# Optimization experiments

Measured on AMD Instinct MI355X. Metric: run time of the kernel, lower is better.

## Reference

```python
import jax, jax.numpy as jnp
import numpy as np

N = 100000        # nodes
E = 1_600_000     # edges (before self loops)
G = 512           # graphs in batch
IN = 64           # in_channels
HID = 48          # hidden_channels
H = 4             # heads
C = HID // H      # per-head channels
OUT = 10          # out_channels


def setup_inputs() -> dict:
    key = jax.random.key(0)
    ks = jax.random.split(key, 24)
    s = 0.1
    inp = {
        "x": jax.random.normal(ks[0], (N, IN), jnp.float32),
        "edge_index": jax.random.randint(ks[1], (2, E), 0, N, dtype=jnp.int64),
        "edge_weight": jax.random.uniform(ks[2], (E,), jnp.float32),
        "batch": jnp.sort(jax.random.randint(ks[3], (N,), 0, G, dtype=jnp.int64)),
        # GATConv layer 0 (IN -> H*C), layers 1,2 (HID -> H*C); bias=False
        "Wg0": jax.random.normal(ks[4], (IN, HID), jnp.float32) * s,
        "as0": jax.random.normal(ks[5], (H, C), jnp.float32) * s,
        "ad0": jax.random.normal(ks[6], (H, C), jnp.float32) * s,
        "Wg1": jax.random.normal(ks[7], (HID, HID), jnp.float32) * s,
        "as1": jax.random.normal(ks[8], (H, C), jnp.float32) * s,
        "ad1": jax.random.normal(ks[9], (H, C), jnp.float32) * s,
        "Wg2": jax.random.normal(ks[10], (HID, HID), jnp.float32) * s,
        "as2": jax.random.normal(ks[11], (H, C), jnp.float32) * s,
        "ad2": jax.random.normal(ks[12], (H, C), jnp.float32) * s,
        # MLP head: Linear(HID,HID) -> BatchNorm -> ReLU -> Linear(HID,OUT)
        "mW1": jax.random.normal(ks[13], (HID, HID), jnp.float32) * s,
        "mb1": jnp.zeros((HID,), jnp.float32),
        "gamma": jnp.ones((HID,), jnp.float32),
        "beta": jnp.zeros((HID,), jnp.float32),
        "mW2": jax.random.normal(ks[14], (HID, OUT), jnp.float32) * s,
        "mb2": jnp.zeros((OUT,), jnp.float32),
    }
    return inp


def _gat_layer(x, src, dst, W, a_src, a_dst):
    # x: [N, F_in] -> per-head features [N, H, C]
    xh = (x @ W).reshape(N, H, C)
    al_s = (xh * a_src).sum(-1)   # [N, H] source attention term
    al_d = (xh * a_dst).sum(-1)   # [N, H] target attention term
    logit = jax.nn.leaky_relu(al_s[src] + al_d[dst], negative_slope=0.2)  # [E', H]
    # segment softmax over incoming edges of each target node
    m = jax.ops.segment_max(logit, dst, num_segments=N)
    e = jnp.exp(logit - m[dst])
    denom = jax.ops.segment_sum(e, dst, num_segments=N)
    alpha = e / (denom[dst] + 1e-16)                     # [E', H]
    msg = xh[src] * alpha[:, :, None]                    # [E', H, C]
    out = jax.ops.segment_sum(msg, dst, num_segments=N)  # [N, H, C]
    return out.reshape(N, H * C)


def reference(x, edge_index, edge_weight, batch, Wg0, as0, ad0, Wg1, as1, ad1,
              Wg2, as2, ad2, mW1, mb1, gamma, beta, mW2, mb2):
    loops = jnp.arange(N, dtype=edge_index.dtype)
    src = jnp.concatenate([edge_index[0], loops])  # add_self_loops=True
    dst = jnp.concatenate([edge_index[1], loops])

    h = jax.nn.relu(_gat_layer(x, src, dst, Wg0, as0, ad0))
    h = jax.nn.relu(_gat_layer(h, src, dst, Wg1, as1, ad1))
    h = jax.nn.relu(_gat_layer(h, src, dst, Wg2, as2, ad2))

    # global mean pool over graph ids
    sums = jax.ops.segment_sum(h, batch, num_segments=G)
    cnt = jax.ops.segment_sum(jnp.ones((N,), h.dtype), batch, num_segments=G)
    g = sums / jnp.maximum(cnt, 1.0)[:, None]            # [G, HID]

    # MLP head (dropout = eval identity; BatchNorm with batch stats)
    z = g @ mW1 + mb1
    mu = z.mean(0)
    var = z.var(0)
    z = (z - mu) * jax.lax.rsqrt(var + 1e-5) * gamma + beta
    z = jax.nn.relu(z)
    last = z @ mW2 + mb2                                 # [G, OUT]

    logp = jax.nn.log_softmax(last, -1)
    soft = jax.nn.softmax(last, -1)  # softmax(log_softmax(x)) == softmax(x)
    return (logp, soft, last)
```

## Files before the change

kernel.cpp:

```cpp
#include <hip/hip_runtime.h>
#include <cstdint>

#define GRAPHS 512
#define HEADS 4
#define CPH 12
#define HID 48
#define NPAIR 24
#define RECW 32
#define OUTC 10
#define WPB 4
#define MAXBUCK 1024
#define ACHUNK 8192
#define BCHUNK 8192

__device__ __forceinline__ float bflo(unsigned u){ return __uint_as_float(u<<16); }
__device__ __forceinline__ float bfhi(unsigned u){ return __uint_as_float(u&0xFFFF0000u); }
__device__ __forceinline__ unsigned pack_bf16(float a, float b){
    unsigned ua=__float_as_uint(a), ub=__float_as_uint(b);
    ua += 0x7FFFu + ((ua>>16)&1u);
    ub += 0x7FFFu + ((ub>>16)&1u);
    return (ua>>16) | (ub & 0xFFFF0000u);
}

template<int FIN, bool BF16IN>
__global__ __launch_bounds__(256) void gemm_al_kernel(
    const void* __restrict__ hin_, const float* __restrict__ W,
    const float* __restrict__ avs, const float* __restrict__ avd,
    unsigned* __restrict__ rec, int n)
{
    const int NPB = 32;
    __shared__ float sW[FIN * HID];
    __shared__ float sH[NPB][FIN + 2];
    __shared__ float sV[NPB][HID + 2];
    __shared__ float sA[HID], sB[HID];

    int t = threadIdx.x;
    for (int i = t; i < FIN * HID; i += 256) sW[i] = W[i];
    if (t < HID) { sA[t] = avs[t]; sB[t] = avd[t]; }

    int base = blockIdx.x * NPB;
    if (BF16IN) {
        const unsigned* hin = (const unsigned*)hin_;
        for (int i = t; i < NPB * (FIN / 2); i += 256) {
            int r = i / (FIN / 2), pc = i % (FIN / 2);
            int node = base + r;
            unsigned u = (node < n) ? hin[(size_t)node * (FIN / 2) + pc] : 0u;
            sH[r][2 * pc]     = bflo(u);
            sH[r][2 * pc + 1] = bfhi(u);
        }
    } else {
        const float* hin = (const float*)hin_;
        for (int i = t; i < NPB * FIN; i += 256) {
            int r = i / FIN, k = i % FIN;
            int node = base + r;
            sH[r][k] = (node < n) ? hin[(size_t)node * FIN + k] : 0.f;
        }
    }
    __syncthreads();

    for (int i = t; i < NPB * NPAIR; i += 256) {
        int r = i / NPAIR, pc = i % NPAIR;
        float a0 = 0.f, a1 = 0.f;
        #pragma unroll
        for (int k = 0; k < FIN; k += 2) {
            float h0 = sH[r][k], h1 = sH[r][k + 1];
            const float* wp = &sW[k * HID + 2 * pc];
            a0 = fmaf(h0, wp[0], a0);       a1 = fmaf(h0, wp[1], a1);
            a0 = fmaf(h1, wp[HID], a0);     a1 = fmaf(h1, wp[HID + 1], a1);
        }
        sV[r][2 * pc] = a0; sV[r][2 * pc + 1] = a1;
        int node = base + r;
        if (node < n) rec[(size_t)node * RECW + 4 + pc] = pack_bf16(a0, a1);
    }
    __syncthreads();

    if (t < NPB * HEADS) {
        int r = t / HEADS, h = t % HEADS;
        int node = base + r;
        if (node < n) {
            float ss = 0.f, dd = 0.f;
            #pragma unroll
            for (int j = 0; j < CPH; ++j) {
                float v = sV[r][h * CPH + j];
                ss = fmaf(v, sA[h * CPH + j], ss);
                dd = fmaf(v, sB[h * CPH + j], dd);
            }
            float* recf = (float*)(rec + (size_t)node * RECW);
            recf[h]      = ss;
            recf[28 + h] = dd;
        }
    }
}

__global__ __launch_bounds__(256) void passA_kernel(
    const int* __restrict__ edst, int E, int* __restrict__ bcnt, int nbuck)
{
    __shared__ int lh[MAXBUCK];
    for (int i = threadIdx.x; i < nbuck; i += 256) lh[i] = 0;
    __syncthreads();
    int e0 = blockIdx.x * ACHUNK, e1 = min(E, e0 + ACHUNK);
    for (int e = e0 + threadIdx.x; e < e1; e += 256)
        atomicAdd(&lh[edst[e] >> 8], 1);
    __syncthreads();
    for (int i = threadIdx.x; i < nbuck; i += 256) {
        int v = lh[i];
        if (v) atomicAdd(&bcnt[i], v);
    }
}

__global__ __launch_bounds__(1024) void bscan_kernel(
    const int* __restrict__ bcnt, int* __restrict__ boff, int nbuck, int etot)
{
    __shared__ int s[1024];
    int t = threadIdx.x;
    int v = (t < nbuck) ? bcnt[t] : 0;
    s[t] = v; __syncthreads();
    for (int off = 1; off < 1024; off <<= 1) {
        int a = (t >= off) ? s[t - off] : 0;
        __syncthreads();
        s[t] += a;
        __syncthreads();
    }
    if (t < nbuck) boff[t] = s[t] - v;
    if (t == 0) boff[nbuck] = etot;
}

__global__ __launch_bounds__(256) void passB_kernel(
    const int* __restrict__ esrc, const int* __restrict__ edst, int E,
    const int* __restrict__ boff, int* __restrict__ gcur,
    unsigned* __restrict__ ebuf, int nbuck)
{
    __shared__ int lcnt[MAXBUCK];
    __shared__ int lbase[MAXBUCK];
    for (int i = threadIdx.x; i < nbuck; i += 256) lcnt[i] = 0;
    __syncthreads();
    int e0 = blockIdx.x * BCHUNK, e1 = min(E, e0 + BCHUNK);
    for (int e = e0 + threadIdx.x; e < e1; e += 256)
        atomicAdd(&lcnt[edst[e] >> 8], 1);
    __syncthreads();
    for (int i = threadIdx.x; i < nbuck; i += 256) {
        int c = lcnt[i];
        lbase[i] = c ? (boff[i] + atomicAdd(&gcur[i], c)) : 0;
        lcnt[i] = 0;
    }
    __syncthreads();
    for (int e = e0 + threadIdx.x; e < e1; e += 256) {
        int d = edst[e], s = esrc[e];
        int b = d >> 8;
        int rk = atomicAdd(&lcnt[b], 1);
        ebuf[lbase[b] + rk] = ((unsigned)(d & 255) << 24) | (unsigned)s;
    }
}

__global__ __launch_bounds__(256) void passC_kernel(
    const unsigned* __restrict__ ebuf, const int* __restrict__ boff,
    int* __restrict__ rowptr, int* __restrict__ colidx, int n, int E)
{
    __shared__ int lcnt[256];
    __shared__ int sc[256];
    __shared__ int lcur[256];
    int b = blockIdx.x, t = threadIdx.x;
    int nbase = b << 8;
    lcnt[t] = 0;
    __syncthreads();
    int s0 = boff[b], s1 = boff[b + 1];
    for (int i = s0 + t; i < s1; i += 256)
        atomicAdd(&lcnt[ebuf[i] >> 24], 1);
    __syncthreads();
    sc[t] = lcnt[t]; __syncthreads();
    for (int off = 1; off < 256; off <<= 1) {
        int v = (t >= off) ? sc[t - off] : 0;
        __syncthreads();
        sc[t] += v;
        __syncthreads();
    }
    int rp = s0 + sc[t] - lcnt[t];
    if (nbase + t < n) rowptr[nbase + t] = rp;
    if (b == (int)gridDim.x - 1 && t == 0) rowptr[n] = E;
    lcur[t] = rp;
    __syncthreads();
    for (int i = s0 + t; i < s1; i += 256) {
        unsigned u = ebuf[i];
        int pos = atomicAdd(&lcur[u >> 24], 1);
        colidx[pos] = (int)(u & 0xFFFFFFu);
    }
}

__global__ __launch_bounds__(256) void agg_kernel(
    const int* __restrict__ rowptr, const int* __restrict__ colidx,
    const unsigned* __restrict__ rec,
    unsigned* __restrict__ hb, int n)
{
    __shared__ float tb[WPB][2][32][5];
    __shared__ int   sb[WPB][2][32];
    const int w = threadIdx.x >> 6, lane = threadIdx.x & 63;
    const int half = lane >> 5, l32 = lane & 31;
    const int node = (blockIdx.x * WPB + w) * 2 + half;
    const bool act = node < n;

    int start = 0, end = 0;
    if (act) { start = rowptr[node]; end = rowptr[node + 1]; }

    const unsigned* nrec = rec + (size_t)node * RECW;
    float4 asn  = act ? *(const float4*)(nrec)      : float4{0.f,0.f,0.f,0.f};
    float4 aldn = act ? *(const float4*)(nrec + 28) : float4{0.f,0.f,0.f,0.f};

    const bool fmaL = l32 < NPAIR;
    const bool denL = (l32 >= NPAIR) && (l32 < NPAIR + 4);
    const int p  = fmaL ? l32 : 0;
    const int hh = denL ? (l32 - NPAIR) : (p / 6);

    float as_h = hh < 2 ? (hh == 0 ? asn.x : asn.y) : (hh == 2 ? asn.z : asn.w);
    float ad_h = hh < 2 ? (hh == 0 ? aldn.x : aldn.y) : (hh == 2 ? aldn.z : aldn.w);
    float ls = as_h + ad_h; ls = ls > 0.f ? ls : 0.2f * ls;
    const float tself = __expf(ls);

    float a0 = 0.f, a1 = 0.f, a2 = 0.f, a3 = 0.f, den = 0.f;
    if (act && fmaL) {
        unsigned u = nrec[4 + p];
        a0 = tself * bflo(u);
        a1 = tself * bfhi(u);
    }
    if (act && denL) den = tself;

    for (int cb = start; cb < end; cb += 32) {
        const int m = min(32, end - cb);
        {
            int idx = cb + l32; if (idx >= end) idx = end - 1;
            int s = colidx[idx];
            sb[w][half][l32] = s;
            float4 a = *(const float4*)(rec + (size_t)s * RECW);
            float l0 = a.x + aldn.x; l0 = l0 > 0.f ? l0 : 0.2f * l0;
            float l1 = a.y + aldn.y; l1 = l1 > 0.f ? l1 : 0.2f * l1;
            float l2 = a.z + aldn.z; l2 = l2 > 0.f ? l2 : 0.2f * l2;
            float l3 = a.w + aldn.w; l3 = l3 > 0.f ? l3 : 0.2f * l3;
            tb[w][half][l32][0] = __expf(l0);
            tb[w][half][l32][1] = __expf(l1);
            tb[w][half][l32][2] = __expf(l2);
            tb[w][half][l32][3] = __expf(l3);
        }
        __builtin_amdgcn_sched_barrier(0);
        if (fmaL) {
            int j = 0;
            for (; j + 2 <= m; j += 2) {
                int s0 = sb[w][half][j], s1 = sb[w][half][j + 1];
                float t0 = tb[w][half][j][hh], t1 = tb[w][half][j + 1][hh];
                unsigned u0 = rec[(size_t)s0 * RECW + 4 + p];
                unsigned u1 = rec[(size_t)s1 * RECW + 4 + p];
                a0 = fmaf(t0, bflo(u0), a0); a1 = fmaf(t0, bfhi(u0), a1);
                a2 = fmaf(t1, bflo(u1), a2); a3 = fmaf(t1, bfhi(u1), a3);
            }
            if (j < m) {
                int s0 = sb[w][half][j];
                float t0 = tb[w][half][j][hh];
                unsigned u0 = rec[(size_t)s0 * RECW + 4 + p];
                a0 = fmaf(t0, bflo(u0), a0); a1 = fmaf(t0, bfhi(u0), a1);
            }
        } else if (denL) {
            for (int j = 0; j < m; ++j) den += tb[w][half][j][hh];
        }
        __builtin_amdgcn_sched_barrier(0);
    }

    float aLo = a0 + a2, aHi = a1 + a3;
    float dd = __shfl(den, half * 32 + NPAIR + hh, 64);
    if (act && fmaL) {
        float inv = 1.f / (dd + 1e-16f);
        float vLo = aLo * inv; vLo = vLo > 0.f ? vLo : 0.f;
        float vHi = aHi * inv; vHi = vHi > 0.f ? vHi : 0.f;
        hb[(size_t)node * NPAIR + p] = pack_bf16(vLo, vHi);
    }
}

__global__ __launch_bounds__(256) void pool_mlp1_kernel(
    const unsigned* __restrict__ hb, const int* __restrict__ batch,
    const float* __restrict__ W1, const float* __restrict__ b1,
    float* __restrict__ z, int n)
{
    __shared__ float sLo[8][NPAIR];
    __shared__ float sHi[8][NPAIR];
    __shared__ float sg[HID];
    int g = blockIdx.x;
    int lo = 0, hi = n;
    while (lo < hi) { int mid = (lo + hi) >> 1; if (batch[mid] < g) lo = mid + 1; else hi = mid; }
    int start = lo;
    lo = start; hi = n;
    while (lo < hi) { int mid = (lo + hi) >> 1; if (batch[mid] < g + 1) lo = mid + 1; else hi = mid; }
    int end = lo;

    int r = threadIdx.x >> 5;
    int p = threadIdx.x & 31;
    if (p < NPAIR) {
        float aLo = 0.f, aHi = 0.f;
        for (int i = start + r; i < end; i += 8) {
            unsigned u = hb[(size_t)i * NPAIR + p];
            aLo += bflo(u); aHi += bfhi(u);
        }
        sLo[r][p] = aLo; sHi[r][p] = aHi;
    }
    __syncthreads();
    if (threadIdx.x < NPAIR) {
        float l = 0.f, h2 = 0.f;
        #pragma unroll
        for (int rr = 0; rr < 8; ++rr) { l += sLo[rr][threadIdx.x]; h2 += sHi[rr][threadIdx.x]; }
        float cnt = (float)(end > start ? end - start : 1);
        sg[2 * threadIdx.x]     = l / cnt;
        sg[2 * threadIdx.x + 1] = h2 / cnt;
    }
    __syncthreads();
    int c = threadIdx.x;
    if (c < HID) {
        float acc = b1[c];
        #pragma unroll
        for (int k = 0; k < HID; ++k) acc = fmaf(sg[k], W1[k * HID + c], acc);
        z[g * HID + c] = acc;
    }
}

__global__ __launch_bounds__(256) void bn_stats_kernel(
    const float* __restrict__ z, float* __restrict__ mu, float* __restrict__ rsig)
{
    int j = blockIdx.x;
    int t = threadIdx.x;
    float s = 0.f, s2 = 0.f;
    for (int i = t; i < GRAPHS; i += 256) {
        float v = z[i * HID + j];
        s += v; s2 += v * v;
    }
    __shared__ float rs[256], rs2[256];
    rs[t] = s; rs2[t] = s2; __syncthreads();
    for (int off = 128; off > 0; off >>= 1) {
        if (t < off) { rs[t] += rs[t + off]; rs2[t] += rs2[t + off]; }
        __syncthreads();
    }
    if (t == 0) {
        float m = rs[0] / GRAPHS;
        float var = rs2[0] / GRAPHS - m * m;
        mu[j] = m;
        rsig[j] = rsqrtf(var + 1e-5f);
    }
}

__global__ __launch_bounds__(64) void head_kernel(
    const float* __restrict__ z, const float* __restrict__ mu, const float* __restrict__ rsig,
    const float* __restrict__ gamma, const float* __restrict__ beta,
    const float* __restrict__ W2, const float* __restrict__ b2,
    float* __restrict__ out)
{
    __shared__ float zn[HID];
    __shared__ float lastv[OUTC];
    __shared__ float red[2];
    int g = blockIdx.x;
    int t = threadIdx.x;
    if (t < HID) {
        float v = (z[g * HID + t] - mu[t]) * rsig[t] * gamma[t] + beta[t];
        zn[t] = v > 0.f ? v : 0.f;
    }
    __syncthreads();
    if (t < OUTC) {
        float acc = b2[t];
        #pragma unroll
        for (int k = 0; k < HID; ++k) acc = fmaf(zn[k], W2[k * OUTC + t], acc);
        lastv[t] = acc;
    }
    __syncthreads();
    if (t == 0) {
        float m = lastv[0];
        for (int o = 1; o < OUTC; ++o) m = fmaxf(m, lastv[o]);
        float se = 0.f;
        for (int o = 0; o < OUTC; ++o) se += expf(lastv[o] - m);
        red[0] = m; red[1] = logf(se);
    }
    __syncthreads();
    if (t < OUTC) {
        float l = lastv[t];
        float lp = l - red[0] - red[1];
        out[g * OUTC + t] = lp;
        out[GRAPHS * OUTC + g * OUTC + t] = expf(lp);
        out[2 * GRAPHS * OUTC + g * OUTC + t] = l;
    }
}

extern "C" void kernel_launch(void* const* d_in, const int* in_sizes, int n_in,
                              void* d_out, int out_size, void* d_ws, size_t ws_size,
                              hipStream_t stream)
{
    const float* x     = (const float*)d_in[0];
    const int*   ei    = (const int*)  d_in[1];
    const int*   batch = (const int*)  d_in[3];
    const float* Wg0 = (const float*)d_in[4];
    const float* as0 = (const float*)d_in[5];
    const float* ad0 = (const float*)d_in[6];
    const float* Wg1 = (const float*)d_in[7];
    const float* as1 = (const float*)d_in[8];
    const float* ad1 = (const float*)d_in[9];
    const float* Wg2 = (const float*)d_in[10];
    const float* as2 = (const float*)d_in[11];
    const float* ad2 = (const float*)d_in[12];
    const float* mW1 = (const float*)d_in[13];
    const float* mb1 = (const float*)d_in[14];
    const float* gamma = (const float*)d_in[15];
    const float* beta  = (const float*)d_in[16];
    const float* mW2 = (const float*)d_in[17];
    const float* mb2 = (const float*)d_in[18];

    const int n  = in_sizes[3];
    const int E  = in_sizes[1] / 2;
    const int FIN0 = in_sizes[0] / n;
    const int nbuck = (n + 255) >> 8;

    unsigned* rec = (unsigned*)d_ws;
    unsigned* hb  = rec + (size_t)n * RECW;
    float* zbuf  = (float*)(hb + (size_t)n * NPAIR);
    float* mu    = zbuf + GRAPHS * HID;
    float* rsig  = mu + HID;
    int* rowptr  = (int*)(rsig + HID);
    int* boff    = rowptr + (n + 1);
    int* bcnt    = boff + (MAXBUCK + 1);
    int* gcur    = bcnt + MAXBUCK;
    unsigned* ebuf = (unsigned*)(gcur + MAXBUCK);
    int* colidx  = (int*)(ebuf + E);

    const int* esrc = ei;
    const int* edst = ei + E;

    hipMemsetAsync(bcnt, 0, 2 * MAXBUCK * sizeof(int), stream);
    passA_kernel<<<(E + ACHUNK - 1) / ACHUNK, 256, 0, stream>>>(edst, E, bcnt, nbuck);
    bscan_kernel<<<1, 1024, 0, stream>>>(bcnt, boff, nbuck, E);
    passB_kernel<<<(E + BCHUNK - 1) / BCHUNK, 256, 0, stream>>>(esrc, edst, E, boff, gcur, ebuf, nbuck);
    passC_kernel<<<nbuck, 256, 0, stream>>>(ebuf, boff, rowptr, colidx, n, E);

    const int gemm_blocks = (n + 31) / 32;
    const int agg_blocks  = (n + 2 * WPB - 1) / (2 * WPB);

    if (FIN0 == 64)
        gemm_al_kernel<64, false><<<gemm_blocks, 256, 0, stream>>>(x, Wg0, as0, ad0, rec, n);
    else
        gemm_al_kernel<48, false><<<gemm_blocks, 256, 0, stream>>>(x, Wg0, as0, ad0, rec, n);
    agg_kernel<<<agg_blocks, 256, 0, stream>>>(rowptr, colidx, rec, hb, n);
    gemm_al_kernel<48, true><<<gemm_blocks, 256, 0, stream>>>(hb, Wg1, as1, ad1, rec, n);
    agg_kernel<<<agg_blocks, 256, 0, stream>>>(rowptr, colidx, rec, hb, n);
    gemm_al_kernel<48, true><<<gemm_blocks, 256, 0, stream>>>(hb, Wg2, as2, ad2, rec, n);
    agg_kernel<<<agg_blocks, 256, 0, stream>>>(rowptr, colidx, rec, hb, n);

    pool_mlp1_kernel<<<GRAPHS, 256, 0, stream>>>(hb, batch, mW1, mb1, zbuf, n);
    bn_stats_kernel<<<HID, 256, 0, stream>>>(zbuf, mu, rsig);
    head_kernel<<<GRAPHS, 64, 0, stream>>>(zbuf, mu, rsig, gamma, beta, mW2, mb2, (float*)d_out);
}
```

Baseline: 440.7 us.

## Register-tile GAT feature GEMM with float4 smem and fused attention dot products

Rewrites the per-layer node GEMM so each thread computes a 4-node by 4-column register tile using float4 shared-memory loads of weights and inputs, with 64 nodes per 192-thread block. The attention source/target terms are computed from the register accumulators and reduced per head through shared-memory atomics, which removes the intermediate sV staging buffer and one sync phase. The aim is to cut shared-memory traffic and instruction count in the GEMM kernels. In exchange it uses more registers per thread and relies on shared float atomics, which make the per-head sums order-dependent.

```diff
diff --git a/kernel.cpp b/kernel.cpp
--- a/kernel.cpp
+++ b/kernel.cpp
@@ -22,72 +22,133 @@
     return (ua>>16) | (ub & 0xFFFF0000u);
 }
 
+__device__ __forceinline__ void fma4(float4& a, const float4 h,
+    const float4 w0, const float4 w1, const float4 w2, const float4 w3)
+{
+    a.x = fmaf(h.x, w0.x, a.x); a.x = fmaf(h.y, w1.x, a.x); a.x = fmaf(h.z, w2.x, a.x); a.x = fmaf(h.w, w3.x, a.x);
+    a.y = fmaf(h.x, w0.y, a.y); a.y = fmaf(h.y, w1.y, a.y); a.y = fmaf(h.z, w2.y, a.y); a.y = fmaf(h.w, w3.y, a.y);
+    a.z = fmaf(h.x, w0.z, a.z); a.z = fmaf(h.y, w1.z, a.z); a.z = fmaf(h.z, w2.z, a.z); a.z = fmaf(h.w, w3.z, a.z);
+    a.w = fmaf(h.x, w0.w, a.w); a.w = fmaf(h.y, w1.w, a.w); a.w = fmaf(h.z, w2.w, a.w); a.w = fmaf(h.w, w3.w, a.w);
+}
+
 template<int FIN, bool BF16IN>
-__global__ __launch_bounds__(256) void gemm_al_kernel(
+__global__ __launch_bounds__(192) void gemm_al_kernel(
     const void* __restrict__ hin_, const float* __restrict__ W,
     const float* __restrict__ avs, const float* __restrict__ avd,
     unsigned* __restrict__ rec, int n)
 {
-    const int NPB = 32;
-    __shared__ float sW[FIN * HID];
-    __shared__ float sH[NPB][FIN + 2];
-    __shared__ float sV[NPB][HID + 2];
+    const int NPB = 64;
+    const int SHW = FIN / 4 + 1;
+    __shared__ float4 sH[NPB * SHW];
+    __shared__ float4 sW4[FIN * 12];
     __shared__ float sA[HID], sB[HID];
-
-    int t = threadIdx.x;
-    for (int i = t; i < FIN * HID; i += 256) sW[i] = W[i];
+    __shared__ float sALS[NPB][HEADS];
+    __shared__ float sALD[NPB][HEADS];
+
+    const int t = threadIdx.x;
+    const int base = blockIdx.x * NPB;
+
+    for (int i = t; i < FIN * 12; i += 192) sW4[i] = ((const float4*)W)[i];
     if (t < HID) { sA[t] = avs[t]; sB[t] = avd[t]; }
-
-    int base = blockIdx.x * NPB;
+    if (t < NPB) {
+        *(float4*)&sALS[t][0] = float4{0.f,0.f,0.f,0.f};
+        *(float4*)&sALD[t][0] = float4{0.f,0.f,0.f,0.f};
+    }
+
     if (BF16IN) {
         const unsigned* hin = (const unsigned*)hin_;
-        for (int i = t; i < NPB * (FIN / 2); i += 256) {
+        float* sHf = (float*)sH;
+        const int RW = 4 * SHW;
+        for (int i = t; i < NPB * (FIN / 2); i += 192) {
             int r = i / (FIN / 2), pc = i % (FIN / 2);
             int node = base + r;
             unsigned u = (node < n) ? hin[(size_t)node * (FIN / 2) + pc] : 0u;
-            sH[r][2 * pc]     = bflo(u);
-            sH[r][2 * pc + 1] = bfhi(u);
+            sHf[r * RW + 2 * pc]     = bflo(u);
+            sHf[r * RW + 2 * pc + 1] = bfhi(u);
         }
     } else {
-        const float* hin = (const float*)hin_;
-        for (int i = t; i < NPB * FIN; i += 256) {
-            int r = i / FIN, k = i % FIN;
+        const float4* hin = (const float4*)hin_;
+        for (int i = t; i < NPB * (FIN / 4); i += 192) {
+            int r = i / (FIN / 4), q = i % (FIN / 4);
             int node = base + r;
-            sH[r][k] = (node < n) ? hin[(size_t)node * FIN + k] : 0.f;
-        }
-    }
-    __syncthreads();
-
-    for (int i = t; i < NPB * NPAIR; i += 256) {
-        int r = i / NPAIR, pc = i % NPAIR;
-        float a0 = 0.f, a1 = 0.f;
-        #pragma unroll
-        for (int k = 0; k < FIN; k += 2) {
-            float h0 = sH[r][k], h1 = sH[r][k + 1];
-            const float* wp = &sW[k * HID + 2 * pc];
-            a0 = fmaf(h0, wp[0], a0);       a1 = fmaf(h0, wp[1], a1);
-            a0 = fmaf(h1, wp[HID], a0);     a1 = fmaf(h1, wp[HID + 1], a1);
-        }
-        sV[r][2 * pc] = a0; sV[r][2 * pc + 1] = a1;
-        int node = base + r;
-        if (node < n) rec[(size_t)node * RECW + 4 + pc] = pack_bf16(a0, a1);
-    }
-    __syncthreads();
-
-    if (t < NPB * HEADS) {
-        int r = t / HEADS, h = t % HEADS;
-        int node = base + r;
+            sH[r * SHW + q] = (node < n) ? hin[(size_t)node * (FIN / 4) + q]
+                                         : float4{0.f,0.f,0.f,0.f};
+        }
+    }
+    __syncthreads();
+
+    const int cs = t >> 4;
+    const int ns = t & 15;
+
+    float4 acc0{0.f,0.f,0.f,0.f}, acc1{0.f,0.f,0.f,0.f};
+    float4 acc2{0.f,0.f,0.f,0.f}, acc3{0.f,0.f,0.f,0.f};
+
+    #pragma unroll
+    for (int kq = 0; kq < FIN / 4; ++kq) {
+        float4 w0 = sW4[(4 * kq + 0) * 12 + cs];
+        float4 w1 = sW4[(4 * kq + 1) * 12 + cs];
+        float4 w2 = sW4[(4 * kq + 2) * 12 + cs];
+        float4 w3 = sW4[(4 * kq + 3) * 12 + cs];
+        float4 h0 = sH[(ns +  0) * SHW + kq];
+        float4 h1 = sH[(ns + 16) * SHW + kq];
+        float4 h2 = sH[(ns + 32) * SHW + kq];
+        float4 h3 = sH[(ns + 48) * SHW + kq];
+        fma4(acc0, h0, w0, w1, w2, w3);
+        fma4(acc1, h1, w0, w1, w2, w3);
+        fma4(acc2, h2, w0, w1, w2, w3);
+        fma4(acc3, h3, w0, w1, w2, w3);
+    }
+
+    const int hh = cs / 3;
+    const float A0 = sA[4*cs], A1 = sA[4*cs+1], A2 = sA[4*cs+2], A3 = sA[4*cs+3];
+    const float B0 = sB[4*cs], B1 = sB[4*cs+1], B2 = sB[4*cs+2], B3 = sB[4*cs+3];
+
+    {
+        float ss, dd;
+        ss = fmaf(acc0.x,A0, fmaf(acc0.y,A1, fmaf(acc0.z,A2, acc0.w*A3)));
+        dd = fmaf(acc0.x,B0, fmaf(acc0.y,B1, fmaf(acc0.z,B2, acc0.w*B3)));
+        atomicAdd(&sALS[ns +  0][hh], ss); atomicAdd(&sALD[ns +  0][hh], dd);
+        ss = fmaf(acc1.x,A0, fmaf(acc1.y,A1, fmaf(acc1.z,A2, acc1.w*A3)));
+        dd = fmaf(acc1.x,B0, fmaf(acc1.y,B1, fmaf(acc1.z,B2, acc1.w*B3)));
+        atomicAdd(&sALS[ns + 16][hh], ss); atomicAdd(&sALD[ns + 16][hh], dd);
+        ss = fmaf(acc2.x,A0, fmaf(acc2.y,A1, fmaf(acc2.z,A2, acc2.w*A3)));
+        dd = fmaf(acc2.x,B0, fmaf(acc2.y,B1, fmaf(acc2.z,B2, acc2.w*B3)));
+        atomicAdd(&sALS[ns + 32][hh], ss); atomicAdd(&sALD[ns + 32][hh], dd);
+        ss = fmaf(acc3.x,A0, fmaf(acc3.y,A1, fmaf(acc3.z,A2, acc3.w*A3)));
+        dd = fmaf(acc3.x,B0, fmaf(acc3.y,B1, fmaf(acc3.z,B2, acc3.w*B3)));
+        atomicAdd(&sALS[ns + 48][hh], ss); atomicAdd(&sALD[ns + 48][hh], dd);
+    }
+
+    {
+        int node = base + ns;
         if (node < n) {
-            float ss = 0.f, dd = 0.f;
-            #pragma unroll
-            for (int j = 0; j < CPH; ++j) {
-                float v = sV[r][h * CPH + j];
-                ss = fmaf(v, sA[h * CPH + j], ss);
-                dd = fmaf(v, sB[h * CPH + j], dd);
-            }
+            unsigned* rp = rec + (size_t)node * RECW + 4 + 2 * cs;
+            rp[0] = pack_bf16(acc0.x, acc0.y); rp[1] = pack_bf16(acc0.z, acc0.w);
+        }
+        node = base + ns + 16;
+        if (node < n) {
+            unsigned* rp = rec + (size_t)node * RECW + 4 + 2 * cs;
+            rp[0] = pack_bf16(acc1.x, acc1.y); rp[1] = pack_bf16(acc1.z, acc1.w);
+        }
+        node = base + ns + 32;
+        if (node < n) {
+            unsigned* rp = rec + (size_t)node * RECW + 4 + 2 * cs;
+            rp[0] = pack_bf16(acc2.x, acc2.y); rp[1] = pack_bf16(acc2.z, acc2.w);
+        }
+        node = base + ns + 48;
+        if (node < n) {
+            unsigned* rp = rec + (size_t)node * RECW + 4 + 2 * cs;
+            rp[0] = pack_bf16(acc3.x, acc3.y); rp[1] = pack_bf16(acc3.z, acc3.w);
+        }
+    }
+
+    __syncthreads();
+    if (t < NPB) {
+        int node = base + t;
+        if (node < n) {
             float* recf = (float*)(rec + (size_t)node * RECW);
-            recf[h]      = ss;
-            recf[28 + h] = dd;
+            *(float4*)recf        = *(float4*)&sALS[t][0];
+            *(float4*)(recf + 28) = *(float4*)&sALD[t][0];
         }
     }
 }
@@ -430,17 +491,17 @@
     passB_kernel<<<(E + BCHUNK - 1) / BCHUNK, 256, 0, stream>>>(esrc, edst, E, boff, gcur, ebuf, nbuck);
     passC_kernel<<<nbuck, 256, 0, stream>>>(ebuf, boff, rowptr, colidx, n, E);
 
-    const int gemm_blocks = (n + 31) / 32;
+    const int gemm_blocks = (n + 63) / 64;
     const int agg_blocks  = (n + 2 * WPB - 1) / (2 * WPB);
 
     if (FIN0 == 64)
-        gemm_al_kernel<64, false><<<gemm_blocks, 256, 0, stream>>>(x, Wg0, as0, ad0, rec, n);
+        gemm_al_kernel<64, false><<<gemm_blocks, 192, 0, stream>>>(x, Wg0, as0, ad0, rec, n);
     else
-        gemm_al_kernel<48, false><<<gemm_blocks, 256, 0, stream>>>(x, Wg0, as0, ad0, rec, n);
+        gemm_al_kernel<48, false><<<gemm_blocks, 192, 0, stream>>>(x, Wg0, as0, ad0, rec, n);
     agg_kernel<<<agg_blocks, 256, 0, stream>>>(rowptr, colidx, rec, hb, n);
-    gemm_al_kernel<48, true><<<gemm_blocks, 256, 0, stream>>>(hb, Wg1, as1, ad1, rec, n);
+    gemm_al_kernel<48, true><<<gemm_blocks, 192, 0, stream>>>(hb, Wg1, as1, ad1, rec, n);
     agg_kernel<<<agg_blocks, 256, 0, stream>>>(rowptr, colidx, rec, hb, n);
-    gemm_al_kernel<48, true><<<gemm_blocks, 256, 0, stream>>>(hb, Wg2, as2, ad2, rec, n);
+    gemm_al_kernel<48, true><<<gemm_blocks, 192, 0, stream>>>(hb, Wg2, as2, ad2, rec, n);
     agg_kernel<<<agg_blocks, 256, 0, stream>>>(rowptr, colidx, rec, hb, n);
 
     pool_mlp1_kernel<<<GRAPHS, 256, 0, stream>>>(hb, batch, mW1, mb1, zbuf, n);
```

After: 421.7 us. -4.3%, faster.
